# Performance work log

Measured on AMD Instinct MI355X. Metric: run time of the kernel, lower is better.

Reference implementation:

```python
import jax, jax.numpy as jnp
import numpy as np

B, S, D = 4, 2048, 512
H = 8
DH = D // H  # depth per head = 64
SCALE = 1.0 / np.sqrt(np.float32(D))  # NOTE: original divides by sqrt(feature_size), not sqrt(depth)
EPS = 1e-5


def setup_inputs() -> dict:
    key = jax.random.key(0)
    ks = jax.random.split(key, 10)
    std = 1.0 / np.sqrt(D)
    inp = {
        "x": jax.random.normal(ks[0], (B, S, D), dtype=jnp.float32),
        "w_q": jax.random.uniform(ks[1], (D, D), jnp.float32, -std, std),
        "b_q": jax.random.uniform(ks[2], (D,), jnp.float32, -std, std),
        "w_k": jax.random.uniform(ks[3], (D, D), jnp.float32, -std, std),
        "b_k": jax.random.uniform(ks[4], (D,), jnp.float32, -std, std),
        "w_v": jax.random.uniform(ks[5], (D, D), jnp.float32, -std, std),
        "b_v": jax.random.uniform(ks[6], (D,), jnp.float32, -std, std),
        "w_o": jax.random.uniform(ks[7], (D, D), jnp.float32, -std, std),
        "b_o": jax.random.uniform(ks[8], (D,), jnp.float32, -std, std),
        "ln_gamma": jnp.ones((D,), jnp.float32),
        "ln_beta": jnp.zeros((D,), jnp.float32),
    }
    return inp


def _split_heads(t):
    # [B, S, D] -> [B, H, S, DH]
    return t.reshape(B, S, H, DH).transpose(0, 2, 1, 3)


def reference(x, w_q, b_q, w_k, b_k, w_v, b_v, w_o, b_o, ln_gamma, ln_beta):
    q = _split_heads(x @ w_q.T + b_q)
    k = _split_heads(x @ w_k.T + b_k)
    v = _split_heads(x @ w_v.T + b_v)
    # scores: [B, H, S, S], scaled by 1/sqrt(feature_size) per the original
    scores = jnp.einsum("bhqd,bhkd->bhqk", q, k) * SCALE
    alpha = jax.nn.softmax(scores, axis=-1)
    context = jnp.einsum("bhqk,bhkd->bhqd", alpha, v)
    context = context.transpose(0, 2, 1, 3).reshape(B, S, D)
    out = context @ w_o.T + b_o
    # residual + LayerNorm
    y = out + x
    mu = jnp.mean(y, axis=-1, keepdims=True)
    var = jnp.mean(jnp.square(y - mu), axis=-1, keepdims=True)
    y = (y - mu) * jax.lax.rsqrt(var + EPS)
    return y * ln_gamma + ln_beta
```

## Files before the change

kernel.cpp:

```cpp
#include <hip/hip_runtime.h>
#include <hip/hip_bf16.h>
#include <math.h>

#define BB 4
#define SS 2048
#define DD 512
#define HH 8
#define DHH 64
#define MROWS (BB*SS)

constexpr float SCALE  = 0.044194173824159216f;
constexpr float QSCALE = (float)(0.044194173824159216 * 1.4426950408889634);
constexpr float LN_EPS = 1e-5f;

typedef __attribute__((ext_vector_type(8)))  short bf16x8;
typedef __attribute__((ext_vector_type(4)))  float f32x4;
typedef __attribute__((ext_vector_type(16))) float f32x16;

__device__ __forceinline__ ushort f2bf(float f) {
    __hip_bfloat16 h = __float2bfloat16(f);
    ushort u; __builtin_memcpy(&u, &h, 2);
    return u;
}

__device__ __forceinline__ float exp2_hw(float x) {
#if __has_builtin(__builtin_amdgcn_exp2f)
    return __builtin_amdgcn_exp2f(x);
#else
    return exp2f(x);
#endif
}

__device__ __forceinline__ unsigned cvt_pk_bf16(float lo, float hi) {
    unsigned r;
    asm("v_cvt_pk_bf16_f32 %0, %1, %2" : "=v"(r) : "v"(lo), "v"(hi));
    return r;
}
__device__ __forceinline__ void plane_swap(unsigned &a, unsigned &b) {
    asm("v_permlane32_swap_b32 %0, %1" : "+v"(a), "+v"(b));
}
__device__ __forceinline__ void plane_swapf(float &a, float &b) {
    asm("v_permlane32_swap_b32 %0, %1" : "+v"(a), "+v"(b));
}
__device__ __forceinline__ bf16x8 pack4(unsigned a0, unsigned a1, unsigned b0, unsigned b1) {
    union { unsigned u[4]; bf16x8 v; } x;
    x.u[0] = a0; x.u[1] = a1; x.u[2] = b0; x.u[3] = b1;
    return x.v;
}

__device__ __forceinline__ void gload16(const void* gsrc, void* lds_dst) {
    __builtin_amdgcn_global_load_lds(
        (const __attribute__((address_space(1))) unsigned int*)gsrc,
        (__attribute__((address_space(3))) unsigned int*)lds_dst,
        16, 0, 0);
}

__global__ __launch_bounds__(256) void cast_kernel(
    const float* __restrict__ x,
    const float* __restrict__ wq, const float* __restrict__ wk,
    const float* __restrict__ wv, const float* __restrict__ wo,
    const float* __restrict__ bq, const float* __restrict__ bk,
    const float* __restrict__ bv,
    ushort* __restrict__ xb, ushort* __restrict__ wb, float* __restrict__ biasc)
{
    const int gid = blockIdx.x * 256 + threadIdx.x;
    if (gid < 1536) {
        float v = gid < 512 ? bq[gid] * QSCALE
                : gid < 1024 ? bk[gid - 512] : bv[gid - 1024];
        biasc[gid] = v;
    }
    const int NX4 = (MROWS * DD) / 4;
    const int NW4 = (DD * DD) / 4;
    const int total = NX4 + 4 * NW4;
    for (int i = gid; i < total; i += gridDim.x * 256) {
        float4 v; ushort4 o;
        if (i < NX4) {
            v = ((const float4*)x)[i];
            o.x = f2bf(v.x); o.y = f2bf(v.y); o.z = f2bf(v.z); o.w = f2bf(v.w);
            ((ushort4*)xb)[i] = o;
        } else {
            int j = i - NX4;
            int which = j >> 16;
            int off = j & 65535;
            const float4* src = which == 0 ? (const float4*)wq
                              : which == 1 ? (const float4*)wk
                              : which == 2 ? (const float4*)wv : (const float4*)wo;
            v = src[off];
            float scl = which == 0 ? QSCALE : 1.0f;
            o.x = f2bf(v.x * scl); o.y = f2bf(v.y * scl);
            o.z = f2bf(v.z * scl); o.w = f2bf(v.w * scl);
            ((ushort4*)wb)[j] = o;
        }
    }
}

__device__ __forceinline__ void stage_tile(const ushort* __restrict__ g, int k0,
                                           ushort* lbuf, int t)
{
    #pragma unroll
    for (int i = 0; i < 4; ++i) {
        int cc = i * 256 + t;
        int row = cc >> 3, slot = cc & 7;
        gload16(g + row * DD + k0 + ((slot ^ (row & 7)) << 3), lbuf + cc * 8);
    }
}

__device__ __forceinline__ void mma_step(const ushort* Abuf, const ushort* Bbuf,
                                         int wr, int wc, int c, int g,
                                         f32x4 (&acc)[4][4])
{
    bf16x8 af[2][4], bf[2][4];
    #pragma unroll
    for (int kc = 0; kc < 2; ++kc) {
        int sw = ((kc * 4 + g) ^ (c & 7)) << 4;
        #pragma unroll
        for (int mi = 0; mi < 4; ++mi)
            af[kc][mi] = *(const bf16x8*)((const char*)Abuf + (wr*64 + mi*16 + c)*128 + sw);
        #pragma unroll
        for (int ni = 0; ni < 4; ++ni)
            bf[kc][ni] = *(const bf16x8*)((const char*)Bbuf + (wc*64 + ni*16 + c)*128 + sw);
    }
    __builtin_amdgcn_s_setprio(1);
    #pragma unroll
    for (int kc = 0; kc < 2; ++kc)
        #pragma unroll
        for (int mi = 0; mi < 4; ++mi)
            #pragma unroll
            for (int ni = 0; ni < 4; ++ni)
                acc[mi][ni] = __builtin_amdgcn_mfma_f32_16x16x32_bf16(
                    af[kc][mi], bf[kc][ni], acc[mi][ni], 0, 0, 0);
    __builtin_amdgcn_s_setprio(0);
}

__global__ __launch_bounds__(256) void qkv_mm(
    const ushort* __restrict__ xb, const ushort* __restrict__ wb,
    const float* __restrict__ biasc,
    ushort* __restrict__ Qb, ushort* __restrict__ Kb, ushort* __restrict__ Vtb)
{
    __shared__ char smem[34816];
    ushort* Abuf = (ushort*)smem;
    ushort* Bbuf = (ushort*)(smem + 16384);

    const int t = threadIdx.x, w = t >> 6, lane = t & 63;
    const int wr = w >> 1, wc = w & 1, c = lane & 15, g = lane >> 4;
    const int nblk = blockIdx.x, mblk = blockIdx.y;

    const ushort* Ag = xb + (size_t)mblk * 128 * DD;
    const ushort* Bg = wb + (size_t)nblk * 128 * DD;

    f32x4 acc[4][4] = {};

    for (int k0 = 0; k0 < DD; k0 += 64) {
        stage_tile(Ag, k0, Abuf, t);
        stage_tile(Bg, k0, Bbuf, t);
        __syncthreads();
        mma_step(Abuf, Bbuf, wr, wc, c, g, acc);
        __syncthreads();
    }

    ushort* E = (ushort*)(smem + (size_t)w * 8704);
    const int n0w  = nblk*128 + wc*64;
    const int proj = n0w >> 9;
    const int h    = (n0w & 511) >> 6;
    const int m0w  = mblk*128 + wr*64;
    const int bi   = m0w >> 11;
    const int st0  = m0w & 2047;

    if (proj == 2) {
        #pragma unroll
        for (int mi = 0; mi < 4; ++mi)
            #pragma unroll
            for (int ni = 0; ni < 4; ++ni) {
                float bias = biasc[n0w + ni*16 + c];
                ushort4 pk = { f2bf(acc[mi][ni][0]+bias), f2bf(acc[mi][ni][1]+bias),
                               f2bf(acc[mi][ni][2]+bias), f2bf(acc[mi][ni][3]+bias) };
                *(ushort4*)&E[(ni*16 + c)*68 + mi*16 + g*4] = pk;
            }
    } else {
        #pragma unroll
        for (int mi = 0; mi < 4; ++mi)
            #pragma unroll
            for (int ni = 0; ni < 4; ++ni) {
                float bias = biasc[n0w + ni*16 + c];
                #pragma unroll
                for (int rg = 0; rg < 4; ++rg)
                    E[(mi*16 + g*4 + rg)*68 + ni*16 + c] = f2bf(acc[mi][ni][rg]+bias);
            }
    }

    const int l = lane;
    if (proj == 0) {
        char* base = (char*)Qb + ((size_t)(bi*HH + h)*64 + (st0 >> 5) + (l >> 5)) * 4096;
        #pragma unroll
        for (int j = 0; j < 8; ++j) {
            uint2 v0 = *(uint2*)&E[l*68 + j*8];
            uint2 v1 = *(uint2*)&E[l*68 + j*8 + 4];
            uint4 v = { v0.x, v0.y, v1.x, v1.y };
            *(uint4*)(base + j*512 + (l & 31)*16) = v;
        }
    } else if (proj == 1) {
        char* base = (char*)Kb + ((size_t)(bi*HH + h)*32 + (st0 >> 6)) * 8192;
        #pragma unroll
        for (int j = 0; j < 8; ++j) {
            uint2 v0 = *(uint2*)&E[l*68 + j*8];
            uint2 v1 = *(uint2*)&E[l*68 + j*8 + 4];
            uint4 v = { v0.x, v0.y, v1.x, v1.y };
            *(uint4*)(base + j*1024 + l*16) = v;
        }
    } else {
        char* base = (char*)Vtb + ((size_t)(bi*HH + h)*32 + (st0 >> 6)) * 8192;
        #pragma unroll
        for (int j = 0; j < 8; ++j) {
            uint2 v0 = *(uint2*)&E[l*68 + j*8];
            uint2 v1 = *(uint2*)&E[l*68 + j*8 + 4];
            uint4 v = { v0.x, v0.y, v1.x, v1.y };
            *(uint4*)(base + j*1024 + l*16) = v;
        }
    }
}

__global__ __launch_bounds__(256) void oproj_mm(
    const ushort* __restrict__ ctx, const ushort* __restrict__ wob,
    const float* __restrict__ bo, const float* __restrict__ resid,
    float* __restrict__ out)
{
    __shared__ ushort Abuf[128*64];
    __shared__ ushort Bbuf[128*64];
    const int t = threadIdx.x, w = t >> 6, lane = t & 63;
    const int wr = w >> 1, wc = w & 1, c = lane & 15, g = lane >> 4;
    const int nblk = blockIdx.x, mblk = blockIdx.y;

    const ushort* Ag = ctx + (size_t)mblk * 128 * DD;
    const ushort* Bg = wob + (size_t)nblk * 128 * DD;

    f32x4 acc[4][4] = {};

    for (int k0 = 0; k0 < DD; k0 += 64) {
        stage_tile(Ag, k0, Abuf, t);
        stage_tile(Bg, k0, Bbuf, t);
        __syncthreads();
        mma_step(Abuf, Bbuf, wr, wc, c, g, acc);
        __syncthreads();
    }

    #pragma unroll
    for (int mi = 0; mi < 4; ++mi) {
        int m = mblk*128 + wr*64 + mi*16 + g*4;
        #pragma unroll
        for (int ni = 0; ni < 4; ++ni) {
            int ng = nblk*128 + wc*64 + ni*16 + c;
            float bias = bo[ng];
            #pragma unroll
            for (int rg = 0; rg < 4; ++rg) {
                int mm = m + rg;
                out[(size_t)mm*DD + ng] = acc[mi][ni][rg] + bias + resid[(size_t)mm*DD + ng];
            }
        }
    }
}

__global__ __launch_bounds__(512, 4) void attn_kernel(
    const ushort* __restrict__ Q, const ushort* __restrict__ K,
    const ushort* __restrict__ Vt, ushort* __restrict__ ctx)
{
    __shared__ ushort Ks[2][2][64*64];
    __shared__ ushort Vts[2][3][64*64];

    const int t = threadIdx.x;
    const int w = t >> 6, l = t & 63;
    const int ln31 = l & 31, hi = l >> 5;
    const int qb = w & 3, kvh = w >> 2;

    const int id  = blockIdx.x;
    const int swz = (id & 7) * 64 + (id >> 3);
    const int qt = swz & 15;
    const int h  = (swz >> 4) & 7;
    const int b  = swz >> 7;
    const size_t bh = (size_t)b * HH + h;
    const int q0 = qt*128 + qb*32;

    const char* Qp = (const char*)Q + (bh*64 + (size_t)(qt*4 + qb)) * 4096;
    bf16x8 qf[4];
    #pragma unroll
    for (int s = 0; s < 4; ++s)
        qf[s] = *(const bf16x8*)(Qp + (2*s + hi)*512 + ln31*16);

    const int t2 = t & 255;
    const int NT = 16;
    const size_t kvbase = bh * 32;

#define ATTN_STAGE(kvi, kb_, vb_) do {                                      \
        const size_t tb_ = (kvbase + (size_t)(kvh*NT + (kvi))) * 8192;      \
        const char* kp_ = (const char*)K  + tb_;                            \
        const char* vp_ = (const char*)Vt + tb_;                            \
        gload16(kp_ + t2*16,        (char*)&Ks[kvh][kb_][0] + t2*16);       \
        gload16(kp_ + 4096 + t2*16, (char*)&Ks[kvh][kb_][0] + 4096 + t2*16);\
        gload16(vp_ + t2*16,        (char*)&Vts[kvh][vb_][0] + t2*16);      \
        gload16(vp_ + 4096 + t2*16, (char*)&Vts[kvh][vb_][0] + 4096 + t2*16);\
    } while (0)

#define QKT(kb_, ST) do {                                                   \
        const char* Kc_ = (const char*)&Ks[kvh][kb_][0];                    \
        __builtin_amdgcn_s_setprio(1);                                      \
        _Pragma("unroll")                                                   \
        for (int kt = 0; kt < 2; ++kt) {                                    \
            f32x16 z_ = {};                                                 \
            _Pragma("unroll")                                               \
            for (int s = 0; s < 4; ++s) {                                   \
                bf16x8 kf_ = *(const bf16x8*)(Kc_ + ((2*s + hi) << 10)      \
                                                  + ((kt*32 + ln31) << 4)); \
                z_ = __builtin_amdgcn_mfma_f32_32x32x16_bf16(kf_, qf[s], z_, 0, 0, 0); \
            }                                                               \
            ST[kt] = z_;                                                    \
        }                                                                   \
        __builtin_amdgcn_s_setprio(0);                                      \
    } while (0)

#define PVSTEP(vb_, PB) do {                                                \
        const char* Vc_ = (const char*)&Vts[kvh][vb_][0];                   \
        __builtin_amdgcn_s_setprio(1);                                      \
        _Pragma("unroll")                                                   \
        for (int kt = 0; kt < 2; ++kt)                                      \
            _Pragma("unroll")                                               \
            for (int s2 = 0; s2 < 2; ++s2)                                  \
                _Pragma("unroll")                                           \
                for (int dt = 0; dt < 2; ++dt) {                            \
                    bf16x8 vf_ = *(const bf16x8*)(Vc_ + ((kt*4 + 2*s2 + hi) << 10) \
                                                      + ((dt*32 + ln31) << 4));    \
                    ot[dt] = __builtin_amdgcn_mfma_f32_32x32x16_bf16(vf_, PB[kt][s2], ot[dt], 0, 0, 0); \
                }                                                           \
        __builtin_amdgcn_s_setprio(0);                                      \
    } while (0)

#define SOFTPACK(ST, PB) do {                                               \
        _Pragma("unroll")                                                   \
        for (int kt = 0; kt < 2; ++kt)                                      \
            _Pragma("unroll")                                               \
            for (int i = 0; i < 16; ++i)                                    \
                ST[kt][i] = exp2_hw(ST[kt][i]);                             \
        {                                                                   \
            float ps_[16];                                                  \
            _Pragma("unroll")                                               \
            for (int i = 0; i < 16; ++i) ps_[i] = ST[0][i] + ST[1][i];      \
            _Pragma("unroll")                                               \
            for (int i = 0; i < 8; ++i)  ps_[i] += ps_[i+8];                \
            _Pragma("unroll")                                               \
            for (int i = 0; i < 4; ++i)  ps_[i] += ps_[i+4];                \
            float psum_ = (ps_[0] + ps_[1]) + (ps_[2] + ps_[3]);            \
            float pa_ = psum_, pb2_ = psum_;                                \
            plane_swapf(pa_, pb2_);                                         \
            lsum += pa_ + pb2_;                                             \
        }                                                                   \
        unsigned dk_[2][4][2];                                              \
        _Pragma("unroll")                                                   \
        for (int kt = 0; kt < 2; ++kt)                                      \
            _Pragma("unroll")                                               \
            for (int rb = 0; rb < 4; ++rb) {                                \
                dk_[kt][rb][0] = cvt_pk_bf16(ST[kt][4*rb+0], ST[kt][4*rb+1]);\
                dk_[kt][rb][1] = cvt_pk_bf16(ST[kt][4*rb+2], ST[kt][4*rb+3]);\
            }                                                               \
        _Pragma("unroll")                                                   \
        for (int kt = 0; kt < 2; ++kt)                                      \
            _Pragma("unroll")                                               \
            for (int s2 = 0; s2 < 2; ++s2) {                                \
                unsigned a0_ = dk_[kt][2*s2][0], b0_ = dk_[kt][2*s2+1][0];  \
                unsigned a1_ = dk_[kt][2*s2][1], b1_ = dk_[kt][2*s2+1][1];  \
                plane_swap(a0_, b0_);                                       \
                plane_swap(a1_, b1_);                                       \
                PB[kt][s2] = pack4(a0_, a1_, b0_, b1_);                     \
            }                                                               \
    } while (0)

#define ITER(kv, PBP, PBC) do {                                             \
        __syncthreads();                                                    \
        if ((kv) + 1 < NT) ATTN_STAGE((kv)+1, ((kv)+1)&1, ((kv)+1)%3);      \
        f32x16 stl[2];                                                      \
        QKT((kv)&1, stl);                                                   \
        PVSTEP(((kv)-1)%3, PBP);                                            \
        SOFTPACK(stl, PBC);                                                 \
    } while (0)

    f32x16 ot[2] = {};
    float lsum = 0.f;
    bf16x8 pbA[2][2], pbB[2][2];

    ATTN_STAGE(0, 0, 0);
    __syncthreads();
    ATTN_STAGE(1, 1, 1);
    {
        f32x16 stl[2];
        QKT(0, stl);
        SOFTPACK(stl, pbA);
    }

    for (int kv = 1; kv <= 13; kv += 2) {
        ITER(kv,     pbA, pbB);
        ITER(kv + 1, pbB, pbA);
    }
    ITER(15, pbA, pbB);
    PVSTEP(15 % 3, pbB);

#undef ITER
#undef SOFTPACK
#undef PVSTEP
#undef QKT
#undef ATTN_STAGE

    __syncthreads();
    float* comb = (float*)&Ks[0][0][0];
    float* p = comb + (size_t)(qb*64 + l) * 33;
    if (kvh == 0) {
        #pragma unroll
        for (int i = 0; i < 16; ++i) { p[i] = ot[0][i]; p[16+i] = ot[1][i]; }
        p[32] = lsum;
    }
    __syncthreads();
    if (kvh == 1) {
        const float rl = 1.f / (lsum + p[32]);
        ushort* outp = ctx + ((size_t)b*SS + q0 + ln31) * DD + h*DHH;
        #pragma unroll
        for (int dt = 0; dt < 2; ++dt)
            #pragma unroll
            for (int rb = 0; rb < 4; ++rb) {
                ushort4 o = { f2bf((ot[dt][4*rb+0] + p[dt*16+4*rb+0])*rl),
                              f2bf((ot[dt][4*rb+1] + p[dt*16+4*rb+1])*rl),
                              f2bf((ot[dt][4*rb+2] + p[dt*16+4*rb+2])*rl),
                              f2bf((ot[dt][4*rb+3] + p[dt*16+4*rb+3])*rl) };
                *(ushort4*)&outp[dt*32 + rb*8 + hi*4] = o;
            }
    }
}

__global__ __launch_bounds__(256) void ln_kernel(
    const float* __restrict__ y, const float* __restrict__ gamma,
    const float* __restrict__ beta, float* __restrict__ out)
{
    const int row = blockIdx.x;
    const int t = threadIdx.x;
    const float* yr = y + (size_t)row * DD;

    float2 v = *(const float2*)&yr[t*2];
    float s  = v.x + v.y;
    float sq = v.x*v.x + v.y*v.y;
    #pragma unroll
    for (int off = 1; off < 64; off <<= 1) {
        s  += __shfl_xor(s,  off);
        sq += __shfl_xor(sq, off);
    }
    __shared__ float ss[4], ssq[4];
    int wv = t >> 6;
    if ((t & 63) == 0) { ss[wv] = s; ssq[wv] = sq; }
    __syncthreads();
    s  = ss[0] + ss[1] + ss[2] + ss[3];
    sq = ssq[0] + ssq[1] + ssq[2] + ssq[3];

    float mean = s * (1.0f / DD);
    float var  = sq * (1.0f / DD) - mean * mean;
    float rstd = rsqrtf(var + LN_EPS);

    float2 g  = *(const float2*)&gamma[t*2];
    float2 be = *(const float2*)&beta[t*2];
    float2 o;
    o.x = (v.x - mean) * rstd * g.x + be.x;
    o.y = (v.y - mean) * rstd * g.y + be.y;
    *(float2*)&out[(size_t)row * DD + t*2] = o;
}

extern "C" void kernel_launch(void* const* d_in, const int* in_sizes, int n_in,
                              void* d_out, int out_size, void* d_ws, size_t ws_size,
                              hipStream_t stream)
{
    const float* x     = (const float*)d_in[0];
    const float* wq    = (const float*)d_in[1];
    const float* bq    = (const float*)d_in[2];
    const float* wk    = (const float*)d_in[3];
    const float* bk    = (const float*)d_in[4];
    const float* wv    = (const float*)d_in[5];
    const float* bv    = (const float*)d_in[6];
    const float* wo    = (const float*)d_in[7];
    const float* bo    = (const float*)d_in[8];
    const float* gamma = (const float*)d_in[9];
    const float* beta  = (const float*)d_in[10];

    char* wsb = (char*)d_ws;
    const size_t MB = 1u << 20;
    ushort* xb    = (ushort*)(wsb + 0*MB);
    ushort* wb    = (ushort*)(wsb + 8*MB);
    float*  biasc = (float* )(wsb + 10*MB);
    ushort* Qb    = (ushort*)(wsb + 11*MB);
    ushort* Kb    = (ushort*)(wsb + 19*MB);
    ushort* Vtb   = (ushort*)(wsb + 27*MB);
    ushort* ctxb  = (ushort*)(wsb + 35*MB);
    float*  ybuf  = (float*)(wsb + 11*MB);

    cast_kernel<<<2048, 256, 0, stream>>>(x, wq, wk, wv, wo, bq, bk, bv,
                                          xb, wb, biasc);
    {
        dim3 grid(12, 64);
        qkv_mm<<<grid, 256, 0, stream>>>(xb, wb, biasc, Qb, Kb, Vtb);
    }
    {
        attn_kernel<<<512, 512, 0, stream>>>(Qb, Kb, Vtb, ctxb);
    }
    {
        dim3 grid(4, 64);
        oproj_mm<<<grid, 256, 0, stream>>>(ctxb, wb + 3*DD*DD, bo, x, ybuf);
    }
    ln_kernel<<<MROWS, 256, 0, stream>>>(ybuf, gamma, beta, (float*)d_out);
}
```

Before: 99.93 us.

## Fuse x cast into QKV GEMM, store bf16 residual output, split attention accumulators

New measurement: 197.8 us. 97.9% more time.

```diff
diff --git a/kernel.cpp b/kernel.cpp
--- a/kernel.cpp
+++ b/kernel.cpp
@@ -55,13 +55,12 @@
         16, 0, 0);
 }
 
-__global__ __launch_bounds__(256) void cast_kernel(
-    const float* __restrict__ x,
+__global__ __launch_bounds__(256) void wcast_kernel(
     const float* __restrict__ wq, const float* __restrict__ wk,
     const float* __restrict__ wv, const float* __restrict__ wo,
     const float* __restrict__ bq, const float* __restrict__ bk,
     const float* __restrict__ bv,
-    ushort* __restrict__ xb, ushort* __restrict__ wb, float* __restrict__ biasc)
+    ushort* __restrict__ wb, float* __restrict__ biasc)
 {
     const int gid = blockIdx.x * 256 + threadIdx.x;
     if (gid < 1536) {
@@ -69,28 +68,18 @@
                 : gid < 1024 ? bk[gid - 512] : bv[gid - 1024];
         biasc[gid] = v;
     }
-    const int NX4 = (MROWS * DD) / 4;
     const int NW4 = (DD * DD) / 4;
-    const int total = NX4 + 4 * NW4;
-    for (int i = gid; i < total; i += gridDim.x * 256) {
-        float4 v; ushort4 o;
-        if (i < NX4) {
-            v = ((const float4*)x)[i];
-            o.x = f2bf(v.x); o.y = f2bf(v.y); o.z = f2bf(v.z); o.w = f2bf(v.w);
-            ((ushort4*)xb)[i] = o;
-        } else {
-            int j = i - NX4;
-            int which = j >> 16;
-            int off = j & 65535;
-            const float4* src = which == 0 ? (const float4*)wq
-                              : which == 1 ? (const float4*)wk
-                              : which == 2 ? (const float4*)wv : (const float4*)wo;
-            v = src[off];
-            float scl = which == 0 ? QSCALE : 1.0f;
-            o.x = f2bf(v.x * scl); o.y = f2bf(v.y * scl);
-            o.z = f2bf(v.z * scl); o.w = f2bf(v.w * scl);
-            ((ushort4*)wb)[j] = o;
-        }
+    for (int j = gid; j < 4 * NW4; j += gridDim.x * 256) {
+        int which = j >> 16;
+        int off = j & 65535;
+        const float4* src = which == 0 ? (const float4*)wq
+                          : which == 1 ? (const float4*)wk
+                          : which == 2 ? (const float4*)wv : (const float4*)wo;
+        float4 v = src[off];
+        float scl = which == 0 ? QSCALE : 1.0f;
+        ushort4 o = { f2bf(v.x * scl), f2bf(v.y * scl),
+                      f2bf(v.z * scl), f2bf(v.w * scl) };
+        ((ushort4*)wb)[j] = o;
     }
 }
 
@@ -102,6 +91,22 @@
         int cc = i * 256 + t;
         int row = cc >> 3, slot = cc & 7;
         gload16(g + row * DD + k0 + ((slot ^ (row & 7)) << 3), lbuf + cc * 8);
+    }
+}
+
+__device__ __forceinline__ void stage_xtile(const float* __restrict__ g, int k0,
+                                            ushort* lbuf, int t)
+{
+    #pragma unroll
+    for (int i = 0; i < 4; ++i) {
+        int cc = i * 256 + t;
+        int row = cc >> 3, slot = cc & 7;
+        const float* src = g + (size_t)row * DD + k0 + ((slot ^ (row & 7)) << 3);
+        float4 a = *(const float4*)src;
+        float4 b = *(const float4*)(src + 4);
+        uint4 v = { cvt_pk_bf16(a.x, a.y), cvt_pk_bf16(a.z, a.w),
+                    cvt_pk_bf16(b.x, b.y), cvt_pk_bf16(b.z, b.w) };
+        *(uint4*)(lbuf + cc * 8) = v;
     }
 }
 
@@ -133,7 +138,7 @@
 }
 
 __global__ __launch_bounds__(256) void qkv_mm(
-    const ushort* __restrict__ xb, const ushort* __restrict__ wb,
+    const float* __restrict__ x, const ushort* __restrict__ wb,
     const float* __restrict__ biasc,
     ushort* __restrict__ Qb, ushort* __restrict__ Kb, ushort* __restrict__ Vtb)
 {
@@ -145,13 +150,13 @@
     const int wr = w >> 1, wc = w & 1, c = lane & 15, g = lane >> 4;
     const int nblk = blockIdx.x, mblk = blockIdx.y;
 
-    const ushort* Ag = xb + (size_t)mblk * 128 * DD;
+    const float*  Ag = x  + (size_t)mblk * 128 * DD;
     const ushort* Bg = wb + (size_t)nblk * 128 * DD;
 
     f32x4 acc[4][4] = {};
 
     for (int k0 = 0; k0 < DD; k0 += 64) {
-        stage_tile(Ag, k0, Abuf, t);
+        stage_xtile(Ag, k0, Abuf, t);
         stage_tile(Bg, k0, Bbuf, t);
         __syncthreads();
         mma_step(Abuf, Bbuf, wr, wc, c, g, acc);
@@ -222,10 +227,12 @@
 __global__ __launch_bounds__(256) void oproj_mm(
     const ushort* __restrict__ ctx, const ushort* __restrict__ wob,
     const float* __restrict__ bo, const float* __restrict__ resid,
-    float* __restrict__ out)
-{
-    __shared__ ushort Abuf[128*64];
-    __shared__ ushort Bbuf[128*64];
+    ushort* __restrict__ out)
+{
+    __shared__ char smem[34816];
+    ushort* Abuf = (ushort*)smem;
+    ushort* Bbuf = (ushort*)(smem + 16384);
+
     const int t = threadIdx.x, w = t >> 6, lane = t & 63;
     const int wr = w >> 1, wc = w & 1, c = lane & 15, g = lane >> 4;
     const int nblk = blockIdx.x, mblk = blockIdx.y;
@@ -243,19 +250,32 @@
         __syncthreads();
     }
 
-    #pragma unroll
-    for (int mi = 0; mi < 4; ++mi) {
-        int m = mblk*128 + wr*64 + mi*16 + g*4;
+    ushort* E = (ushort*)(smem + (size_t)w * 8704);
+    const int n0w = nblk*128 + wc*64;
+    const int m0w = mblk*128 + wr*64;
+
+    #pragma unroll
+    for (int mi = 0; mi < 4; ++mi)
         #pragma unroll
         for (int ni = 0; ni < 4; ++ni) {
-            int ng = nblk*128 + wc*64 + ni*16 + c;
-            float bias = bo[ng];
+            float bias = bo[n0w + ni*16 + c];
             #pragma unroll
             for (int rg = 0; rg < 4; ++rg) {
-                int mm = m + rg;
-                out[(size_t)mm*DD + ng] = acc[mi][ni][rg] + bias + resid[(size_t)mm*DD + ng];
+                int mm = m0w + mi*16 + g*4 + rg;
+                float val = acc[mi][ni][rg] + bias
+                          + resid[(size_t)mm*DD + n0w + ni*16 + c];
+                E[(mi*16 + g*4 + rg)*68 + ni*16 + c] = f2bf(val);
             }
         }
+
+    const int l = lane;
+    #pragma unroll
+    for (int j = 0; j < 8; ++j) {
+        int row = j*8 + (l >> 3);
+        uint2 v0 = *(uint2*)&E[row*68 + (l & 7)*8];
+        uint2 v1 = *(uint2*)&E[row*68 + (l & 7)*8 + 4];
+        uint4 v = { v0.x, v0.y, v1.x, v1.y };
+        *(uint4*)&out[(size_t)(m0w + row)*DD + n0w + (l & 7)*8] = v;
     }
 }
 
@@ -316,7 +336,7 @@
         __builtin_amdgcn_s_setprio(0);                                      \
     } while (0)
 
-#define PVSTEP(vb_, PB) do {                                                \
+#define PVSTEP(vb_, PB, OT) do {                                            \
         const char* Vc_ = (const char*)&Vts[kvh][vb_][0];                   \
         __builtin_amdgcn_s_setprio(1);                                      \
         _Pragma("unroll")                                                   \
@@ -327,7 +347,7 @@
                 for (int dt = 0; dt < 2; ++dt) {                            \
                     bf16x8 vf_ = *(const bf16x8*)(Vc_ + ((kt*4 + 2*s2 + hi) << 10) \
                                                       + ((dt*32 + ln31) << 4));    \
-                    ot[dt] = __builtin_amdgcn_mfma_f32_32x32x16_bf16(vf_, PB[kt][s2], ot[dt], 0, 0, 0); \
+                    OT[dt] = __builtin_amdgcn_mfma_f32_32x32x16_bf16(vf_, PB[kt][s2], OT[dt], 0, 0, 0); \
                 }                                                           \
         __builtin_amdgcn_s_setprio(0);                                      \
     } while (0)
@@ -371,16 +391,17 @@
             }                                                               \
     } while (0)
 
-#define ITER(kv, PBP, PBC) do {                                             \
+#define ITER(kv, PBP, PBC, OT) do {                                         \
         __syncthreads();                                                    \
         if ((kv) + 1 < NT) ATTN_STAGE((kv)+1, ((kv)+1)&1, ((kv)+1)%3);      \
         f32x16 stl[2];                                                      \
         QKT((kv)&1, stl);                                                   \
-        PVSTEP(((kv)-1)%3, PBP);                                            \
+        PVSTEP(((kv)-1)%3, PBP, OT);                                        \
         SOFTPACK(stl, PBC);                                                 \
     } while (0)
 
-    f32x16 ot[2] = {};
+    f32x16 otA[2] = {};
+    f32x16 otB[2] = {};
     float lsum = 0.f;
     bf16x8 pbA[2][2], pbB[2][2];
 
@@ -394,11 +415,11 @@
     }
 
     for (int kv = 1; kv <= 13; kv += 2) {
-        ITER(kv,     pbA, pbB);
-        ITER(kv + 1, pbB, pbA);
-    }
-    ITER(15, pbA, pbB);
-    PVSTEP(15 % 3, pbB);
+        ITER(kv,     pbA, pbB, otA);
+        ITER(kv + 1, pbB, pbA, otB);
+    }
+    ITER(15, pbA, pbB, otA);
+    PVSTEP(15 % 3, pbB, otB);
 
 #undef ITER
 #undef SOFTPACK
@@ -406,8 +427,12 @@
 #undef QKT
 #undef ATTN_STAGE
 
+    f32x16 ot[2];
+    ot[0] = otA[0] + otB[0];
+    ot[1] = otA[1] + otB[1];
+
     __syncthreads();
-    float* comb = (float*)&Ks[0][0][0];
+    float* comb = (float*)&Vts[0][0][0];
     float* p = comb + (size_t)(qb*64 + l) * 33;
     if (kvh == 0) {
         #pragma unroll
@@ -432,14 +457,18 @@
 }
 
 __global__ __launch_bounds__(256) void ln_kernel(
-    const float* __restrict__ y, const float* __restrict__ gamma,
+    const ushort* __restrict__ y, const float* __restrict__ gamma,
     const float* __restrict__ beta, float* __restrict__ out)
 {
     const int row = blockIdx.x;
     const int t = threadIdx.x;
-    const float* yr = y + (size_t)row * DD;
-
-    float2 v = *(const float2*)&yr[t*2];
+
+    unsigned u = *(const unsigned*)&y[(size_t)row * DD + t*2];
+    union { unsigned u; float f; } lo, hi;
+    lo.u = (u & 0xFFFFu) << 16;
+    hi.u = u & 0xFFFF0000u;
+    float2 v = { lo.f, hi.f };
+
     float s  = v.x + v.y;
     float sq = v.x*v.x + v.y*v.y;
     #pragma unroll
@@ -484,20 +513,18 @@
 
     char* wsb = (char*)d_ws;
     const size_t MB = 1u << 20;
-    ushort* xb    = (ushort*)(wsb + 0*MB);
+    ushort* ybuf  = (ushort*)(wsb + 0*MB);
     ushort* wb    = (ushort*)(wsb + 8*MB);
     float*  biasc = (float* )(wsb + 10*MB);
     ushort* Qb    = (ushort*)(wsb + 11*MB);
     ushort* Kb    = (ushort*)(wsb + 19*MB);
     ushort* Vtb   = (ushort*)(wsb + 27*MB);
     ushort* ctxb  = (ushort*)(wsb + 35*MB);
-    float*  ybuf  = (float*)(wsb + 11*MB);
-
-    cast_kernel<<<2048, 256, 0, stream>>>(x, wq, wk, wv, wo, bq, bk, bv,
-                                          xb, wb, biasc);
+
+    wcast_kernel<<<512, 256, 0, stream>>>(wq, wk, wv, wo, bq, bk, bv, wb, biasc);
     {
         dim3 grid(12, 64);
-        qkv_mm<<<grid, 256, 0, stream>>>(xb, wb, biasc, Qb, Kb, Vtb);
+        qkv_mm<<<grid, 256, 0, stream>>>(x, wb, biasc, Qb, Kb, Vtb);
     }
     {
         attn_kernel<<<512, 512, 0, stream>>>(Qb, Kb, Vtb, ctxb);
```
